# Optimization experiments

Hardware: AMD Instinct MI355X
Metric: run time of the kernel (lower is better)

The kernel has to match this reference:

```python
import jax, jax.numpy as jnp
import numpy as np

B, D_IN, H = 16384, 512, 1024


def setup_inputs() -> dict:
    key = jax.random.key(0)
    ks = jax.random.split(key, 12)
    s_in = 1.0 / np.sqrt(D_IN)
    s_h = 1.0 / np.sqrt(H)
    d = {
        "input_x": jax.random.normal(ks[0], (B, D_IN), jnp.float32),
        "h_old": jax.random.normal(ks[1], (B, H), jnp.float32),
        "c_old": jax.random.normal(ks[2], (B, H), jnp.float32),
    }
    names_U = ["Ui", "Uf", "Uo", "Uc"]
    names_W = ["Wi", "Wf", "Wo", "Wc"]
    for i, n in enumerate(names_U):
        d[n + "_w"] = jax.random.normal(ks[3 + i], (D_IN, H), jnp.float32) * s_in
        d[n + "_b"] = jnp.zeros((H,), jnp.float32)
    for i, n in enumerate(names_W):
        d[n + "_w"] = jax.random.normal(ks[7 + i], (H, H), jnp.float32) * s_h
        d[n + "_b"] = jnp.zeros((H,), jnp.float32)
    return d


def reference(input_x, h_old, c_old,
              Ui_w, Ui_b, Wi_w, Wi_b,
              Uf_w, Uf_b, Wf_w, Wf_b,
              Uo_w, Uo_b, Wo_w, Wo_b,
              Uc_w, Uc_b, Wc_w, Wc_b):
    # Fuse the 8 small GEMMs into 2: concatenate gate projections along the
    # output dim (math identical to 8 separate Dense layers + adds).
    U = jnp.concatenate([Ui_w, Uf_w, Uo_w, Uc_w], axis=1)   # [D_in, 4H]
    W = jnp.concatenate([Wi_w, Wf_w, Wo_w, Wc_w], axis=1)   # [H, 4H]
    b = jnp.concatenate([Ui_b + Wi_b, Uf_b + Wf_b, Uo_b + Wo_b, Uc_b + Wc_b])
    gates = input_x @ U + h_old @ W + b                      # [B, 4H]
    i_t, f_t, o_t, g_t = jnp.split(gates, 4, axis=1)
    i_t = jax.nn.sigmoid(i_t)
    f_t = jax.nn.sigmoid(f_t)
    o_t = jax.nn.sigmoid(o_t)
    c_t = jnp.tanh(g_t)
    c = i_t * c_t + f_t * c_old
    h_new = o_t * jnp.tanh(c)
    return (h_new, c)
```

## Files before the change

### kernel.cpp

```cpp
#include <hip/hip_runtime.h>
#include <hip/hip_bf16.h>
#include <stdint.h>

#define B_ROWS 16384
#define D_IN   512
#define H_DIM  1024
#define K_TOT  1536
#define NT     24
#define NIT    12

typedef __attribute__((ext_vector_type(8))) short  bf16x8;
typedef __attribute__((ext_vector_type(4))) float  f32x4;
typedef __attribute__((ext_vector_type(4))) float  float4v;
typedef __attribute__((ext_vector_type(8))) unsigned short u16x8;

__device__ __forceinline__ unsigned short f2bf(float f) {
    uint32_t u = __float_as_uint(f);
    u = (u + 0x7FFFu + ((u >> 16) & 1u)) >> 16;
    return (unsigned short)u;
}

__global__ void cvt_A(const float* __restrict__ x, const float* __restrict__ h,
                      unsigned short* __restrict__ A) {
    int t   = blockIdx.x * blockDim.x + threadIdx.x;
    int row = t / 192;
    int seg = t % 192;
    const float* src;
    if (seg < 64) src = x + (size_t)row * D_IN + seg * 8;
    else          src = h + (size_t)row * H_DIM + (seg - 64) * 8;
    float4v v0 = *(const float4v*)(src);
    float4v v1 = *(const float4v*)(src + 4);
    u16x8 o;
    o[0] = f2bf(v0[0]); o[1] = f2bf(v0[1]); o[2] = f2bf(v0[2]); o[3] = f2bf(v0[3]);
    o[4] = f2bf(v1[0]); o[5] = f2bf(v1[1]); o[6] = f2bf(v1[2]); o[7] = f2bf(v1[3]);
    *(u16x8*)(A + (size_t)row * K_TOT + seg * 8) = o;
}

__global__ void cvt_B(const float* __restrict__ Ui, const float* __restrict__ Uf,
                      const float* __restrict__ Uo, const float* __restrict__ Uc,
                      const float* __restrict__ Wi, const float* __restrict__ Wf,
                      const float* __restrict__ Wo, const float* __restrict__ Wc,
                      unsigned short* __restrict__ Bg) {
    int t  = blockIdx.x * blockDim.x + threadIdx.x;
    int c  = t / 192;
    int k8 = t % 192;
    int g  = (c >> 4) & 3;
    int h  = ((c >> 6) << 4) | (c & 15);
    const float* up = (g == 0) ? Ui : (g == 1) ? Uf : (g == 2) ? Uo : Uc;
    const float* wp = (g == 0) ? Wi : (g == 1) ? Wf : (g == 2) ? Wo : Wc;
    int k = k8 * 8;
    u16x8 o;
    if (k < 512) {
        const float* s = up + (size_t)k * H_DIM + h;
        #pragma unroll
        for (int i = 0; i < 8; ++i) o[i] = f2bf(s[(size_t)i * H_DIM]);
    } else {
        const float* s = wp + (size_t)(k - 512) * H_DIM + h;
        #pragma unroll
        for (int i = 0; i < 8; ++i) o[i] = f2bf(s[(size_t)i * H_DIM]);
    }
    *(u16x8*)(Bg + (size_t)c * K_TOT + k) = o;
}

__global__ void cvt_bias(const float* __restrict__ Uib, const float* __restrict__ Ufb,
                         const float* __restrict__ Uob, const float* __restrict__ Ucb,
                         const float* __restrict__ Wib, const float* __restrict__ Wfb,
                         const float* __restrict__ Wob, const float* __restrict__ Wcb,
                         float* __restrict__ bias) {
    int t = blockIdx.x * blockDim.x + threadIdx.x;
    int g = t >> 10, h = t & 1023;
    const float* ub = (g == 0) ? Uib : (g == 1) ? Ufb : (g == 2) ? Uob : Ucb;
    const float* wb = (g == 0) ? Wib : (g == 1) ? Wfb : (g == 2) ? Wob : Wcb;
    bias[t] = ub[h] + wb[h];
}

__global__ __launch_bounds__(512, 2) void lstm_gemm(
        const unsigned short* __restrict__ Ag, const unsigned short* __restrict__ Bg,
        const float* __restrict__ bias, const float* __restrict__ c_old,
        float* __restrict__ out) {
    __shared__ __align__(1024) char lds[131072];

    const int tid = threadIdx.x;
    const int l   = tid & 63;
    const int wv  = tid >> 6;
    const int wr  = wv >> 2;
    const int wcn = wv & 3;

    const int orig = blockIdx.x;
    const int wg   = (orig & 7) * 128 + (orig >> 3);
    const int bm   = wg & 63;
    const int bn   = wg >> 6;

    const int Lx   = (l & 7) ^ (l >> 3);
    const int kel  = (Lx & 3) * 8;
    const int rloc = (l >> 3) * 2 + (Lx >> 2);
    const int rr0  = (wv * 2 + 0) * 16 + rloc;
    const int rr1  = (wv * 2 + 1) * 16 + rloc;
    const unsigned short* aS0 = Ag + (size_t)(bm * 256 + rr0) * K_TOT + kel;
    const unsigned short* aS1 = Ag + (size_t)(bm * 256 + rr1) * K_TOT + kel;
    const unsigned short* bS0 = Bg + (size_t)(bn * 256 + rr0) * K_TOT + kel;
    const unsigned short* bS1 = Bg + (size_t)(bn * 256 + rr1) * K_TOT + kel;

    int aoff[8], boff[4];
    #pragma unroll
    for (int m = 0; m < 8; ++m) {
        int ra = wr * 128 + m * 16 + (l & 15);
        aoff[m] = (ra >> 1) * 128 + ((((ra & 1) * 4 + (l >> 4)) ^ ((ra >> 1) & 7)) << 4);
    }
    #pragma unroll
    for (int n = 0; n < 4; ++n) {
        int rb = wcn * 64 + n * 16 + (l & 15);
        boff[n] = (rb >> 1) * 128 + ((((rb & 1) * 4 + (l >> 4)) ^ ((rb >> 1) & 7)) << 4);
    }

#define STAGE(MAT, TILE, Q, BUF) do {                                               \
    const unsigned short* _s0 = ((MAT) ? bS0 : aS0) + ((TILE) * 64 + (Q) * 32);     \
    const unsigned short* _s1 = ((MAT) ? bS1 : aS1) + ((TILE) * 64 + (Q) * 32);     \
    char* _d = (char*)lds + (BUF) * 65536 + (MAT) * 32768 + (Q) * 16384 + wv * 2048;\
    __builtin_amdgcn_global_load_lds(                                               \
        (const __attribute__((address_space(1))) void*)_s0,                         \
        (__attribute__((address_space(3))) void*)_d, 16, 0, 0);                     \
    __builtin_amdgcn_global_load_lds(                                               \
        (const __attribute__((address_space(1))) void*)_s1,                         \
        (__attribute__((address_space(3))) void*)(_d + 1024), 16, 0, 0);            \
} while (0)

    f32x4 acc[8][4] = {};
    bf16x8 bfr[4];

#define PHASE(BUF, Q, H, READB, SMAT, STILE, SQ, SBUF, DOVM) do {                   \
    const char* _ab = (const char*)lds + (BUF) * 65536 + (Q) * 16384;               \
    bf16x8 _a0 = *(const bf16x8*)(_ab + aoff[(H) * 4 + 0]);                         \
    bf16x8 _a1 = *(const bf16x8*)(_ab + aoff[(H) * 4 + 1]);                         \
    bf16x8 _a2 = *(const bf16x8*)(_ab + aoff[(H) * 4 + 2]);                         \
    bf16x8 _a3 = *(const bf16x8*)(_ab + aoff[(H) * 4 + 3]);                         \
    if (READB) {                                                                    \
        const char* _bb = _ab + 32768;                                              \
        bfr[0] = *(const bf16x8*)(_bb + boff[0]);                                   \
        bfr[1] = *(const bf16x8*)(_bb + boff[1]);                                   \
        bfr[2] = *(const bf16x8*)(_bb + boff[2]);                                   \
        bfr[3] = *(const bf16x8*)(_bb + boff[3]);                                   \
    }                                                                               \
    STAGE(SMAT, STILE, SQ, SBUF);                                                   \
    __builtin_amdgcn_s_setprio(1);                                                  \
    acc[(H)*4+0][0] = __builtin_amdgcn_mfma_f32_16x16x32_bf16(_a0, bfr[0], acc[(H)*4+0][0], 0, 0, 0); \
    acc[(H)*4+0][1] = __builtin_amdgcn_mfma_f32_16x16x32_bf16(_a0, bfr[1], acc[(H)*4+0][1], 0, 0, 0); \
    acc[(H)*4+0][2] = __builtin_amdgcn_mfma_f32_16x16x32_bf16(_a0, bfr[2], acc[(H)*4+0][2], 0, 0, 0); \
    acc[(H)*4+0][3] = __builtin_amdgcn_mfma_f32_16x16x32_bf16(_a0, bfr[3], acc[(H)*4+0][3], 0, 0, 0); \
    acc[(H)*4+1][0] = __builtin_amdgcn_mfma_f32_16x16x32_bf16(_a1, bfr[0], acc[(H)*4+1][0], 0, 0, 0); \
    acc[(H)*4+1][1] = __builtin_amdgcn_mfma_f32_16x16x32_bf16(_a1, bfr[1], acc[(H)*4+1][1], 0, 0, 0); \
    acc[(H)*4+1][2] = __builtin_amdgcn_mfma_f32_16x16x32_bf16(_a1, bfr[2], acc[(H)*4+1][2], 0, 0, 0); \
    acc[(H)*4+1][3] = __builtin_amdgcn_mfma_f32_16x16x32_bf16(_a1, bfr[3], acc[(H)*4+1][3], 0, 0, 0); \
    acc[(H)*4+2][0] = __builtin_amdgcn_mfma_f32_16x16x32_bf16(_a2, bfr[0], acc[(H)*4+2][0], 0, 0, 0); \
    acc[(H)*4+2][1] = __builtin_amdgcn_mfma_f32_16x16x32_bf16(_a2, bfr[1], acc[(H)*4+2][1], 0, 0, 0); \
    acc[(H)*4+2][2] = __builtin_amdgcn_mfma_f32_16x16x32_bf16(_a2, bfr[2], acc[(H)*4+2][2], 0, 0, 0); \
    acc[(H)*4+2][3] = __builtin_amdgcn_mfma_f32_16x16x32_bf16(_a2, bfr[3], acc[(H)*4+2][3], 0, 0, 0); \
    acc[(H)*4+3][0] = __builtin_amdgcn_mfma_f32_16x16x32_bf16(_a3, bfr[0], acc[(H)*4+3][0], 0, 0, 0); \
    acc[(H)*4+3][1] = __builtin_amdgcn_mfma_f32_16x16x32_bf16(_a3, bfr[1], acc[(H)*4+3][1], 0, 0, 0); \
    acc[(H)*4+3][2] = __builtin_amdgcn_mfma_f32_16x16x32_bf16(_a3, bfr[2], acc[(H)*4+3][2], 0, 0, 0); \
    acc[(H)*4+3][3] = __builtin_amdgcn_mfma_f32_16x16x32_bf16(_a3, bfr[3], acc[(H)*4+3][3], 0, 0, 0); \
    __builtin_amdgcn_s_setprio(0);                                                  \
    if (DOVM) { asm volatile("s_waitcnt vmcnt(8)\ns_barrier" ::: "memory"); }       \
    else      { asm volatile("s_barrier" ::: "memory"); }                           \
} while (0)

    STAGE(0, 0, 0, 0); STAGE(1, 0, 0, 0);
    STAGE(0, 0, 1, 0); STAGE(1, 0, 1, 0);
    STAGE(0, 1, 0, 1); STAGE(1, 1, 0, 1);
    asm volatile("s_waitcnt vmcnt(8)\ns_barrier" ::: "memory");

    #pragma unroll 1
    for (int i = 0; i < NIT; ++i) {
        const int t1 = 2 * i + 1;
        int t2 = 2 * i + 2; if (t2 >= NT) t2 = 0;
        int t3 = 2 * i + 3; if (t3 >= NT) t3 = 0;
        PHASE(0, 0, 0, 1, 0, t1, 1, 1, 0);
        PHASE(0, 0, 1, 0, 1, t1, 1, 1, 1);
        PHASE(0, 1, 0, 1, 0, t2, 0, 0, 0);
        PHASE(0, 1, 1, 0, 1, t2, 0, 0, 1);
        PHASE(1, 0, 0, 1, 0, t2, 1, 0, 0);
        PHASE(1, 0, 1, 0, 1, t2, 1, 0, 1);
        PHASE(1, 1, 0, 1, 0, t3, 0, 1, 0);
        PHASE(1, 1, 1, 0, 1, t3, 0, 1, 1);
    }

    const int hh  = (bn * 4 + wcn) * 16 + (l & 15);
    const float bi  = bias[hh];
    const float bff = bias[1024 + hh];
    const float bo  = bias[2048 + hh];
    const float bc  = bias[3072 + hh];

    #pragma unroll
    for (int m = 0; m < 8; ++m) {
        const int rb = bm * 256 + wr * 128 + m * 16 + ((l >> 4) * 4);
        #pragma unroll
        for (int j = 0; j < 4; ++j) {
            const int r = rb + j;
            float iv = acc[m][0][j] + bi;
            float fv = acc[m][1][j] + bff;
            float ov = acc[m][2][j] + bo;
            float gv = acc[m][3][j] + bc;
            float it = 1.f / (1.f + __expf(-iv));
            float ft = 1.f / (1.f + __expf(-fv));
            float ot = 1.f / (1.f + __expf(-ov));
            float gt = 1.f - 2.f / (1.f + __expf(2.f * gv));
            float co = c_old[(size_t)r * H_DIM + hh];
            float cn = it * gt + ft * co;
            float th = 1.f - 2.f / (1.f + __expf(2.f * cn));
            out[(size_t)r * H_DIM + hh]                            = ot * th;
            out[(size_t)B_ROWS * H_DIM + (size_t)r * H_DIM + hh]   = cn;
        }
    }
#undef PHASE
#undef STAGE
}

extern "C" void kernel_launch(void* const* d_in, const int* in_sizes, int n_in,
                              void* d_out, int out_size, void* d_ws, size_t ws_size,
                              hipStream_t stream) {
    const float* x  = (const float*)d_in[0];
    const float* h0 = (const float*)d_in[1];
    const float* c0 = (const float*)d_in[2];
    const float* Uw[4] = {(const float*)d_in[3],  (const float*)d_in[5],
                          (const float*)d_in[7],  (const float*)d_in[9]};
    const float* Ub[4] = {(const float*)d_in[4],  (const float*)d_in[6],
                          (const float*)d_in[8],  (const float*)d_in[10]};
    const float* Ww[4] = {(const float*)d_in[11], (const float*)d_in[13],
                          (const float*)d_in[15], (const float*)d_in[17]};
    const float* Wb[4] = {(const float*)d_in[12], (const float*)d_in[14],
                          (const float*)d_in[16], (const float*)d_in[18]};

    unsigned short* Ag = (unsigned short*)d_ws;
    unsigned short* Bg = Ag + (size_t)B_ROWS * K_TOT;
    float* bias        = (float*)(Bg + (size_t)4096 * K_TOT);
    float* out         = (float*)d_out;

    cvt_A<<<12288, 256, 0, stream>>>(x, h0, Ag);
    cvt_B<<<3072, 256, 0, stream>>>(Uw[0], Uw[1], Uw[2], Uw[3],
                                    Ww[0], Ww[1], Ww[2], Ww[3], Bg);
    cvt_bias<<<16, 256, 0, stream>>>(Ub[0], Ub[1], Ub[2], Ub[3],
                                     Wb[0], Wb[1], Wb[2], Wb[3], bias);
    lstm_gemm<<<1024, 512, 0, stream>>>(Ag, Bg, bias, c0, out);
}
```

Baseline: 295.4 us.

## Restructure GEMM LDS layout to row-halves with finer vmcnt waits and new tile mapping

Reorganizes the LDS staging so each stage loads a half of the tile rows across the full 64-wide K slice instead of a K quarter, changes the per-phase work to a 4x2 MFMA quadrant with both K halves, and loosens the wait points to vmcnt(6)/vmcnt(8) at different phases. The block-to-tile mapping is also changed to group blocks per XCD into 4x32 patches for L2 locality. This aims to let compute start after fewer outstanding loads and improve cache reuse, at the cost of more LDS reads per phase (B fragments reloaded each phase) and tricky pipelining correctness.

New measurement: 289.3 us. 2.1% less time.

```diff
diff --git a/kernel.cpp b/kernel.cpp
--- a/kernel.cpp
+++ b/kernel.cpp
@@ -87,36 +87,46 @@
     const int wcn = wv & 3;
 
     const int orig = blockIdx.x;
-    const int wg   = (orig & 7) * 128 + (orig >> 3);
-    const int bm   = wg & 63;
-    const int bn   = wg >> 6;
-
-    const int Lx   = (l & 7) ^ (l >> 3);
-    const int kel  = (Lx & 3) * 8;
-    const int rloc = (l >> 3) * 2 + (Lx >> 2);
-    const int rr0  = (wv * 2 + 0) * 16 + rloc;
-    const int rr1  = (wv * 2 + 1) * 16 + rloc;
-    const unsigned short* aS0 = Ag + (size_t)(bm * 256 + rr0) * K_TOT + kel;
-    const unsigned short* aS1 = Ag + (size_t)(bm * 256 + rr1) * K_TOT + kel;
-    const unsigned short* bS0 = Bg + (size_t)(bn * 256 + rr0) * K_TOT + kel;
-    const unsigned short* bS1 = Bg + (size_t)(bn * 256 + rr1) * K_TOT + kel;
-
-    int aoff[8], boff[4];
+    const int xcd  = orig & 7;
+    const int jj   = orig >> 3;
+    const int bn   = (xcd & 3) * 4 + (jj & 3);
+    const int bm   = (xcd >> 2) * 32 + (jj >> 2);
+
+    const int kg   = (l & 7) ^ (l >> 3);
+    const int rel0 = wv * 16 + (l >> 3);
+    const int rel1 = rel0 + 8;
+    const int rA0 = ((rel0 >> 6) << 7) + (rel0 & 63);
+    const int rA1 = ((rel1 >> 6) << 7) + (rel1 & 63);
+    const int rB0 = ((rel0 >> 5) << 6) + (rel0 & 31);
+    const int rB1 = ((rel1 >> 5) << 6) + (rel1 & 31);
+    const unsigned short* aP0 = Ag + (size_t)(bm * 256 + rA0) * K_TOT + kg * 8;
+    const unsigned short* aP1 = Ag + (size_t)(bm * 256 + rA1) * K_TOT + kg * 8;
+    const unsigned short* bP0 = Bg + (size_t)(bn * 256 + rB0) * K_TOT + kg * 8;
+    const unsigned short* bP1 = Bg + (size_t)(bn * 256 + rB1) * K_TOT + kg * 8;
+
+    const int slot = ((l >> 4) ^ (l & 7)) << 4;
+    int aoffb[8], boffb[4];
     #pragma unroll
-    for (int m = 0; m < 8; ++m) {
-        int ra = wr * 128 + m * 16 + (l & 15);
-        aoff[m] = (ra >> 1) * 128 + ((((ra & 1) * 4 + (l >> 4)) ^ ((ra >> 1) & 7)) << 4);
-    }
+    for (int mq = 0; mq < 2; ++mq)
+        #pragma unroll
+        for (int mm = 0; mm < 4; ++mm) {
+            int pr = mq * 128 + wr * 64 + mm * 16 + (l & 15);
+            aoffb[mq * 4 + mm] = pr * 128 + slot;
+        }
     #pragma unroll
-    for (int n = 0; n < 4; ++n) {
-        int rb = wcn * 64 + n * 16 + (l & 15);
-        boff[n] = (rb >> 1) * 128 + ((((rb & 1) * 4 + (l >> 4)) ^ ((rb >> 1) & 7)) << 4);
-    }
-
-#define STAGE(MAT, TILE, Q, BUF) do {                                               \
-    const unsigned short* _s0 = ((MAT) ? bS0 : aS0) + ((TILE) * 64 + (Q) * 32);     \
-    const unsigned short* _s1 = ((MAT) ? bS1 : aS1) + ((TILE) * 64 + (Q) * 32);     \
-    char* _d = (char*)lds + (BUF) * 65536 + (MAT) * 32768 + (Q) * 16384 + wv * 2048;\
+    for (int nq = 0; nq < 2; ++nq)
+        #pragma unroll
+        for (int nn = 0; nn < 2; ++nn) {
+            int pr = nq * 128 + wcn * 32 + nn * 16 + (l & 15);
+            boffb[nq * 2 + nn] = pr * 128 + slot;
+        }
+
+#define STAGE(MAT, TILE, HF, BUF) do {                                              \
+    const unsigned short* _s0 = ((MAT) ? bP0 : aP0)                                 \
+        + (size_t)((HF) * ((MAT) ? 32 : 64)) * K_TOT + (TILE) * 64;                 \
+    const unsigned short* _s1 = ((MAT) ? bP1 : aP1)                                 \
+        + (size_t)((HF) * ((MAT) ? 32 : 64)) * K_TOT + (TILE) * 64;                 \
+    char* _d = (char*)lds + (BUF) * 65536 + (MAT) * 32768 + (HF) * 16384 + wv * 2048;\
     __builtin_amdgcn_global_load_lds(                                               \
         (const __attribute__((address_space(1))) void*)_s0,                         \
         (__attribute__((address_space(3))) void*)_d, 16, 0, 0);                     \
@@ -126,62 +136,64 @@
 } while (0)
 
     f32x4 acc[8][4] = {};
-    bf16x8 bfr[4];
-
-#define PHASE(BUF, Q, H, READB, SMAT, STILE, SQ, SBUF, DOVM) do {                   \
-    const char* _ab = (const char*)lds + (BUF) * 65536 + (Q) * 16384;               \
-    bf16x8 _a0 = *(const bf16x8*)(_ab + aoff[(H) * 4 + 0]);                         \
-    bf16x8 _a1 = *(const bf16x8*)(_ab + aoff[(H) * 4 + 1]);                         \
-    bf16x8 _a2 = *(const bf16x8*)(_ab + aoff[(H) * 4 + 2]);                         \
-    bf16x8 _a3 = *(const bf16x8*)(_ab + aoff[(H) * 4 + 3]);                         \
-    if (READB) {                                                                    \
-        const char* _bb = _ab + 32768;                                              \
-        bfr[0] = *(const bf16x8*)(_bb + boff[0]);                                   \
-        bfr[1] = *(const bf16x8*)(_bb + boff[1]);                                   \
-        bfr[2] = *(const bf16x8*)(_bb + boff[2]);                                   \
-        bfr[3] = *(const bf16x8*)(_bb + boff[3]);                                   \
-    }                                                                               \
-    STAGE(SMAT, STILE, SQ, SBUF);                                                   \
+
+#define PHASE(BUF, MQ, NQ, SMAT, STILE, SHF, SBUF, WAITK) do {                      \
+    const char* _Ab = (const char*)lds + (BUF) * 65536;                             \
+    const char* _Bb = _Ab + 32768;                                                  \
+    bf16x8 a00 = *(const bf16x8*)(_Ab + (aoffb[(MQ)*4+0]));                         \
+    bf16x8 a01 = *(const bf16x8*)(_Ab + (aoffb[(MQ)*4+1]));                         \
+    bf16x8 a02 = *(const bf16x8*)(_Ab + (aoffb[(MQ)*4+2]));                         \
+    bf16x8 a03 = *(const bf16x8*)(_Ab + (aoffb[(MQ)*4+3]));                         \
+    bf16x8 a10 = *(const bf16x8*)(_Ab + (aoffb[(MQ)*4+0] ^ 64));                    \
+    bf16x8 a11 = *(const bf16x8*)(_Ab + (aoffb[(MQ)*4+1] ^ 64));                    \
+    bf16x8 a12 = *(const bf16x8*)(_Ab + (aoffb[(MQ)*4+2] ^ 64));                    \
+    bf16x8 a13 = *(const bf16x8*)(_Ab + (aoffb[(MQ)*4+3] ^ 64));                    \
+    bf16x8 b00 = *(const bf16x8*)(_Bb + (boffb[(NQ)*2+0]));                         \
+    bf16x8 b01 = *(const bf16x8*)(_Bb + (boffb[(NQ)*2+1]));                         \
+    bf16x8 b10 = *(const bf16x8*)(_Bb + (boffb[(NQ)*2+0] ^ 64));                    \
+    bf16x8 b11 = *(const bf16x8*)(_Bb + (boffb[(NQ)*2+1] ^ 64));                    \
+    STAGE(SMAT, STILE, SHF, SBUF);                                                  \
     __builtin_amdgcn_s_setprio(1);                                                  \
-    acc[(H)*4+0][0] = __builtin_amdgcn_mfma_f32_16x16x32_bf16(_a0, bfr[0], acc[(H)*4+0][0], 0, 0, 0); \
-    acc[(H)*4+0][1] = __builtin_amdgcn_mfma_f32_16x16x32_bf16(_a0, bfr[1], acc[(H)*4+0][1], 0, 0, 0); \
-    acc[(H)*4+0][2] = __builtin_amdgcn_mfma_f32_16x16x32_bf16(_a0, bfr[2], acc[(H)*4+0][2], 0, 0, 0); \
-    acc[(H)*4+0][3] = __builtin_amdgcn_mfma_f32_16x16x32_bf16(_a0, bfr[3], acc[(H)*4+0][3], 0, 0, 0); \
-    acc[(H)*4+1][0] = __builtin_amdgcn_mfma_f32_16x16x32_bf16(_a1, bfr[0], acc[(H)*4+1][0], 0, 0, 0); \
-    acc[(H)*4+1][1] = __builtin_amdgcn_mfma_f32_16x16x32_bf16(_a1, bfr[1], acc[(H)*4+1][1], 0, 0, 0); \
-    acc[(H)*4+1][2] = __builtin_amdgcn_mfma_f32_16x16x32_bf16(_a1, bfr[2], acc[(H)*4+1][2], 0, 0, 0); \
-    acc[(H)*4+1][3] = __builtin_amdgcn_mfma_f32_16x16x32_bf16(_a1, bfr[3], acc[(H)*4+1][3], 0, 0, 0); \
-    acc[(H)*4+2][0] = __builtin_amdgcn_mfma_f32_16x16x32_bf16(_a2, bfr[0], acc[(H)*4+2][0], 0, 0, 0); \
-    acc[(H)*4+2][1] = __builtin_amdgcn_mfma_f32_16x16x32_bf16(_a2, bfr[1], acc[(H)*4+2][1], 0, 0, 0); \
-    acc[(H)*4+2][2] = __builtin_amdgcn_mfma_f32_16x16x32_bf16(_a2, bfr[2], acc[(H)*4+2][2], 0, 0, 0); \
-    acc[(H)*4+2][3] = __builtin_amdgcn_mfma_f32_16x16x32_bf16(_a2, bfr[3], acc[(H)*4+2][3], 0, 0, 0); \
-    acc[(H)*4+3][0] = __builtin_amdgcn_mfma_f32_16x16x32_bf16(_a3, bfr[0], acc[(H)*4+3][0], 0, 0, 0); \
-    acc[(H)*4+3][1] = __builtin_amdgcn_mfma_f32_16x16x32_bf16(_a3, bfr[1], acc[(H)*4+3][1], 0, 0, 0); \
-    acc[(H)*4+3][2] = __builtin_amdgcn_mfma_f32_16x16x32_bf16(_a3, bfr[2], acc[(H)*4+3][2], 0, 0, 0); \
-    acc[(H)*4+3][3] = __builtin_amdgcn_mfma_f32_16x16x32_bf16(_a3, bfr[3], acc[(H)*4+3][3], 0, 0, 0); \
+    acc[(MQ)*4+0][(NQ)*2+0] = __builtin_amdgcn_mfma_f32_16x16x32_bf16(a00, b00, acc[(MQ)*4+0][(NQ)*2+0], 0, 0, 0); \
+    acc[(MQ)*4+0][(NQ)*2+1] = __builtin_amdgcn_mfma_f32_16x16x32_bf16(a00, b01, acc[(MQ)*4+0][(NQ)*2+1], 0, 0, 0); \
+    acc[(MQ)*4+1][(NQ)*2+0] = __builtin_amdgcn_mfma_f32_16x16x32_bf16(a01, b00, acc[(MQ)*4+1][(NQ)*2+0], 0, 0, 0); \
+    acc[(MQ)*4+1][(NQ)*2+1] = __builtin_amdgcn_mfma_f32_16x16x32_bf16(a01, b01, acc[(MQ)*4+1][(NQ)*2+1], 0, 0, 0); \
+    acc[(MQ)*4+2][(NQ)*2+0] = __builtin_amdgcn_mfma_f32_16x16x32_bf16(a02, b00, acc[(MQ)*4+2][(NQ)*2+0], 0, 0, 0); \
+    acc[(MQ)*4+2][(NQ)*2+1] = __builtin_amdgcn_mfma_f32_16x16x32_bf16(a02, b01, acc[(MQ)*4+2][(NQ)*2+1], 0, 0, 0); \
+    acc[(MQ)*4+3][(NQ)*2+0] = __builtin_amdgcn_mfma_f32_16x16x32_bf16(a03, b00, acc[(MQ)*4+3][(NQ)*2+0], 0, 0, 0); \
+    acc[(MQ)*4+3][(NQ)*2+1] = __builtin_amdgcn_mfma_f32_16x16x32_bf16(a03, b01, acc[(MQ)*4+3][(NQ)*2+1], 0, 0, 0); \
+    acc[(MQ)*4+0][(NQ)*2+0] = __builtin_amdgcn_mfma_f32_16x16x32_bf16(a10, b10, acc[(MQ)*4+0][(NQ)*2+0], 0, 0, 0); \
+    acc[(MQ)*4+0][(NQ)*2+1] = __builtin_amdgcn_mfma_f32_16x16x32_bf16(a10, b11, acc[(MQ)*4+0][(NQ)*2+1], 0, 0, 0); \
+    acc[(MQ)*4+1][(NQ)*2+0] = __builtin_amdgcn_mfma_f32_16x16x32_bf16(a11, b10, acc[(MQ)*4+1][(NQ)*2+0], 0, 0, 0); \
+    acc[(MQ)*4+1][(NQ)*2+1] = __builtin_amdgcn_mfma_f32_16x16x32_bf16(a11, b11, acc[(MQ)*4+1][(NQ)*2+1], 0, 0, 0); \
+    acc[(MQ)*4+2][(NQ)*2+0] = __builtin_amdgcn_mfma_f32_16x16x32_bf16(a12, b10, acc[(MQ)*4+2][(NQ)*2+0], 0, 0, 0); \
+    acc[(MQ)*4+2][(NQ)*2+1] = __builtin_amdgcn_mfma_f32_16x16x32_bf16(a12, b11, acc[(MQ)*4+2][(NQ)*2+1], 0, 0, 0); \
+    acc[(MQ)*4+3][(NQ)*2+0] = __builtin_amdgcn_mfma_f32_16x16x32_bf16(a13, b10, acc[(MQ)*4+3][(NQ)*2+0], 0, 0, 0); \
+    acc[(MQ)*4+3][(NQ)*2+1] = __builtin_amdgcn_mfma_f32_16x16x32_bf16(a13, b11, acc[(MQ)*4+3][(NQ)*2+1], 0, 0, 0); \
     __builtin_amdgcn_s_setprio(0);                                                  \
-    if (DOVM) { asm volatile("s_waitcnt vmcnt(8)\ns_barrier" ::: "memory"); }       \
-    else      { asm volatile("s_barrier" ::: "memory"); }                           \
+    if ((WAITK) == 6)      { asm volatile("s_waitcnt vmcnt(6)\ns_barrier" ::: "memory"); } \
+    else if ((WAITK) == 8) { asm volatile("s_waitcnt vmcnt(8)\ns_barrier" ::: "memory"); } \
+    else                   { asm volatile("s_barrier" ::: "memory"); }              \
 } while (0)
 
     STAGE(0, 0, 0, 0); STAGE(1, 0, 0, 0);
-    STAGE(0, 0, 1, 0); STAGE(1, 0, 1, 0);
+    STAGE(1, 0, 1, 0); STAGE(0, 0, 1, 0);
     STAGE(0, 1, 0, 1); STAGE(1, 1, 0, 1);
     asm volatile("s_waitcnt vmcnt(8)\ns_barrier" ::: "memory");
 
     #pragma unroll 1
     for (int i = 0; i < NIT; ++i) {
         const int t1 = 2 * i + 1;
-        int t2 = 2 * i + 2; if (t2 >= NT) t2 = 0;
-        int t3 = 2 * i + 3; if (t3 >= NT) t3 = 0;
-        PHASE(0, 0, 0, 1, 0, t1, 1, 1, 0);
-        PHASE(0, 0, 1, 0, 1, t1, 1, 1, 1);
-        PHASE(0, 1, 0, 1, 0, t2, 0, 0, 0);
-        PHASE(0, 1, 1, 0, 1, t2, 0, 0, 1);
-        PHASE(1, 0, 0, 1, 0, t2, 1, 0, 0);
-        PHASE(1, 0, 1, 0, 1, t2, 1, 0, 1);
-        PHASE(1, 1, 0, 1, 0, t3, 0, 1, 0);
-        PHASE(1, 1, 1, 0, 1, t3, 0, 1, 1);
+        int t2 = 2 * i + 2; if (t2 >= NT) t2 -= NT;
+        int t3 = 2 * i + 3; if (t3 >= NT) t3 -= NT;
+        PHASE(0, 0, 0,  0, t1, 1, 1,  6);
+        PHASE(0, 0, 1,  1, t1, 1, 1,  0);
+        PHASE(0, 1, 0,  0, t2, 0, 0,  0);
+        PHASE(0, 1, 1,  1, t2, 0, 0,  8);
+        PHASE(1, 0, 0,  0, t2, 1, 0,  6);
+        PHASE(1, 0, 1,  1, t2, 1, 0,  0);
+        PHASE(1, 1, 0,  0, t3, 0, 1,  0);
+        PHASE(1, 1, 1,  1, t3, 0, 1,  8);
     }
 
     const int hh  = (bn * 4 + wcn) * 16 + (l & 15);
```
